# Optimization experiments

Measured on AMD Instinct MI355X. Metric: run time of the kernel, lower is better.

## Reference

```python
import jax, jax.numpy as jnp
from jax import lax
import numpy as np

KS = 3          # kernel_size
PAD = 1         # padding of conv_offset
N = KS * KS     # sampling points per pixel
B, C, H, W = 8, 64, 96, 96
OUTC = 64


def setup_inputs() -> dict:
    key = jax.random.key(0)
    k1, k2, k3 = jax.random.split(key, 3)
    x = jax.random.normal(k1, (B, C, H, W), dtype=jnp.float32)
    # conv_offset: Conv2d(C, 2N, ks=3, pad=1); small init so offsets are modest
    w_off = jax.random.normal(k2, (2 * N, C, KS, KS), dtype=jnp.float32) * 0.01
    b_off = jnp.zeros((2 * N,), jnp.float32)
    # conv_kernel: Conv2d(C, OUTC, ks=3, stride=3)
    w_ker = jax.random.normal(k3, (OUTC, C, KS, KS), dtype=jnp.float32) * (1.0 / np.sqrt(C * KS * KS))
    b_ker = jnp.zeros((OUTC,), jnp.float32)
    return {"x": x, "w_off": w_off, "b_off": b_off, "w_ker": w_ker, "b_ker": b_ker}


def _deform_conv(x, w_off, b_off, w_ker, b_ker):
    b, c, h, w = x.shape
    dn = ('NCHW', 'OIHW', 'NCHW')
    # offset field: (b, 2N, h, w); channels [:N] are x(row) offsets, [N:] are y(col)
    offset = lax.conv_general_dilated(x, w_off, (1, 1), [(PAD, PAD), (PAD, PAD)],
                                      dimension_numbers=dn) + b_off[None, :, None, None]
    r = jnp.arange(-(KS - 1) // 2, (KS - 1) // 2 + 1)
    pnx, pny = jnp.meshgrid(r, r, indexing='ij')          # kernel grid offsets p_n
    gx, gy = jnp.meshgrid(jnp.arange(h), jnp.arange(w), indexing='ij')  # p_0
    px = gx[None, None].astype(x.dtype) + pnx.reshape(1, N, 1, 1).astype(x.dtype) + offset[:, :N]
    py = gy[None, None].astype(x.dtype) + pny.reshape(1, N, 1, 1).astype(x.dtype) + offset[:, N:]
    # Bilinear sampling with zero outside the grid. This is exactly the dense
    # G @ x of the original (only the 4 neighbors of p have nonzero G weight).
    x0 = jnp.floor(px); y0 = jnp.floor(py)
    lx = px - x0; ly = py - y0            # grads flow to offsets through lx/ly
    x0i = lax.stop_gradient(x0).astype(jnp.int32)
    y0i = lax.stop_gradient(y0).astype(jnp.int32)
    x_flat = x.transpose(0, 2, 3, 1).reshape(b, h * w, c)  # (b, HW, c)

    def corner(xi, yi, wt):
        valid = ((xi >= 0) & (xi < h) & (yi >= 0) & (yi < w)).astype(x.dtype)
        idx = (jnp.clip(xi, 0, h - 1) * w + jnp.clip(yi, 0, w - 1)).reshape(b, -1)
        g = jax.vmap(lambda im, ix: im[ix])(x_flat, idx)   # (b, N*h*w, c)
        return g * (wt * valid).reshape(b, -1, 1)

    val = (corner(x0i,     y0i,     (1 - lx) * (1 - ly))
           + corner(x0i + 1, y0i,     lx * (1 - ly))
           + corner(x0i,     y0i + 1, (1 - lx) * ly)
           + corner(x0i + 1, y0i + 1, lx * ly))            # (b, N*h*w, c)
    xo = val.reshape(b, N, h, w, c).transpose(0, 4, 2, 3, 1)        # (b,c,h,w,N)
    # _reshape_x_offset: N -> (kr,kc) tiled into (h*ks, w*ks)
    xo = xo.reshape(b, c, h, w, KS, KS).transpose(0, 1, 2, 4, 3, 5).reshape(b, c, h * KS, w * KS)
    out = lax.conv_general_dilated(xo, w_ker, (KS, KS), 'VALID',
                                   dimension_numbers=dn) + b_ker[None, :, None, None]
    return out  # (b, OUTC, h, w)


def reference(x, w_off, b_off, w_ker, b_ker):
    return _deform_conv(x, w_off, b_off, w_ker, b_ker)
```

## Files before the change

kernel.cpp:

```cpp
#include <hip/hip_runtime.h>

#define H_ 96
#define W_ 96
#define HW 9216
#define C_ 64
#define OUTC 64
#define NPTS 9
#define NCH 18
#define B_ 8
#define NPIX 73728

#define PCH 72

typedef __attribute__((ext_vector_type(8))) short short8;
typedef __attribute__((ext_vector_type(4))) float f32x4;
typedef __attribute__((ext_vector_type(4))) unsigned int uint4v;

__device__ __forceinline__ short f2bf(float f) {
    union { float f; unsigned u; } v; v.f = f;
    unsigned r = v.u + 0x7fffu + ((v.u >> 16) & 1u);
    return (short)(r >> 16);
}
__device__ __forceinline__ float bflo(unsigned d) {
    union { unsigned u; float f; } v; v.u = d << 16; return v.f;
}
__device__ __forceinline__ float bfhi(unsigned d) {
    union { unsigned u; float f; } v; v.u = d & 0xffff0000u; return v.f;
}

__global__ __launch_bounds__(256) void prep_xpose(
    const float* __restrict__ x, const float* __restrict__ w_ker,
    const float* __restrict__ w_off, short* __restrict__ x_t,
    short* __restrict__ wk_frag, short* __restrict__ woff_frag)
{
    int blk = blockIdx.x;
    int t   = threadIdx.x;
    if (blk < 576) {
        int b   = blk & 7;
        int sub = blk >> 3;
        int cb  = t & 7;
        int px  = sub * 128 + (t >> 3) * 4;

        const float* xp = x + ((size_t)(b * C_ + cb * 8) * HW) + px;
        f32x4 tl[8];
#pragma unroll
        for (int e = 0; e < 8; ++e) tl[e] = *(const f32x4*)(xp + (size_t)e * HW);
#pragma unroll
        for (int p = 0; p < 4; ++p) {
            short8 s;
#pragma unroll
            for (int e = 0; e < 8; ++e) s[e] = f2bf(tl[e][p]);
            *(short8*)(x_t + ((size_t)(b * HW + px + p) * 64) + cb * 8) = s;
        }
    } else {
        int idx = (blk - 576) * 256 + t;
        if (idx < 36864) {
            int j = idx & 7, l = (idx >> 3) & 63, nt = (idx >> 9) & 3, sg = idx >> 11;
            int q2 = sg & 1, n = sg >> 1;
            int c  = q2 * 32 + ((l >> 4) << 3) + j;
            int oc = nt * 16 + (l & 15);
            wk_frag[idx] = f2bf(w_ker[(oc * C_ + c) * 9 + n]);
        } else {
            int k = idx - 36864;
            int j = k & 7, l = (k >> 3) & 63, nt = (k >> 9) & 1, sg = k >> 10;
            int q2 = sg & 1, n = sg >> 1;
            int c  = q2 * 32 + ((l >> 4) << 3) + j;
            int oc = nt * 16 + (l & 15);
            woff_frag[k] = (oc < NCH) ? f2bf(w_off[(oc * C_ + c) * 9 + n]) : (short)0;
        }
    }
}

__global__ __launch_bounds__(256, 6) void deform_fused(
    const short* __restrict__ x_t, const short* __restrict__ woff_frag,
    const float* __restrict__ b_off, const short* __restrict__ wk_frag,
    const float* __restrict__ b_ker, float* __restrict__ out)
{
    __shared__ __align__(16) short sX[100 * PCH];
    __shared__ float  sE[64 * 20];
    __shared__ float2 sP[16 * 9];

    int t    = threadIdx.x;
    int lane = t & 63;
    int wv   = t >> 6;
    int b    = blockIdx.x & 7;
    int strip= blockIdx.x >> 3;
    int px0  = strip * 16;
    int i    = px0 / W_;
    int j0   = px0 - i * W_;
    int pxl  = lane & 15, kq = lane >> 4;
    int j    = j0 + pxl;
    const short* xb = x_t + (size_t)b * HW * 64;
    const short8 Z8 = {0,0,0,0,0,0,0,0};

    for (int u = t; u < 800; u += 256) {
        int cb = u & 7, rc = u >> 3;
        int r = rc / 20, c = rc - r * 20;
        int row = min(max(i - 2 + r, 0), H_ - 1);
        int col = min(max(j0 - 2 + c, 0), W_ - 1);
        *(short8*)&sX[rc * PCH + cb * 8] =
            *(const short8*)(xb + (row * W_ + col) * 64 + cb * 8);
    }
    __syncthreads();

    f32x4 pa0 = {0,0,0,0}, pa1 = {0,0,0,0};
    auto p1tap = [&](int n) {
        int di = n / 3 - 1, dj = n % 3 - 1;
        int ii = i + di, jj = j + dj;
        bool ok = (ii >= 0) & (ii < H_) & (jj >= 0) & (jj < W_);
        int rc = (di + 2) * 20 + (pxl + dj + 2);
#pragma unroll
        for (int q2 = 0; q2 < 2; ++q2) {
            short8 a = *(const short8*)&sX[rc * PCH + q2 * 32 + kq * 8];
            a = ok ? a : Z8;
            const short* wb = woff_frag + ((n * 2 + q2) * 2) * 512 + lane * 8;
            short8 b0 = *(const short8*)(wb);
            short8 b1 = *(const short8*)(wb + 512);
            pa0 = __builtin_amdgcn_mfma_f32_16x16x32_bf16(a, b0, pa0, 0, 0, 0);
            pa1 = __builtin_amdgcn_mfma_f32_16x16x32_bf16(a, b1, pa1, 0, 0, 0);
        }
    };
    if      (wv == 0) { p1tap(0); p1tap(1); }
    else if (wv == 1) { p1tap(2); p1tap(3); }
    else if (wv == 2) { p1tap(4); p1tap(5); }
    else              { p1tap(6); p1tap(7); p1tap(8); }
    {
        int col = lane & 15, rq = lane >> 4;
#pragma unroll
        for (int r = 0; r < 4; ++r)
            sE[(wv * 16 + rq * 4 + r) * 20 + col] = pa0[r];
        if (col < 2) {
#pragma unroll
            for (int r = 0; r < 4; ++r)
                sE[(wv * 16 + rq * 4 + r) * 20 + 16 + col] = pa1[r];
        }
    }
    __syncthreads();

    if (t < 144) {
        int p = t / 9, n = t - p * 9;
        float ox = sE[p * 20 + n]             + sE[(16 + p) * 20 + n]
                 + sE[(32 + p) * 20 + n]      + sE[(48 + p) * 20 + n]      + b_off[n];
        float oy = sE[p * 20 + 9 + n]         + sE[(16 + p) * 20 + 9 + n]
                 + sE[(32 + p) * 20 + 9 + n]  + sE[(48 + p) * 20 + 9 + n]  + b_off[9 + n];
        sP[p * 9 + n] = make_float2(ox, oy);
    }
    __syncthreads();

    f32x4 acc[4];
#pragma unroll
    for (int nt = 0; nt < 4; ++nt) acc[nt] = (f32x4){0.f, 0.f, 0.f, 0.f};

    auto p2tap = [&](int n) {
        int di = n / 3 - 1, dj = n % 3 - 1;
        float2 o = sP[pxl * 9 + n];
        float fpx = (float)(i + di) + o.x;
        float fpy = (float)(j + dj) + o.y;
        float x0f = floorf(fpx), y0f = floorf(fpy);
        float lx = fpx - x0f, ly = fpy - y0f;
        int xi = (int)x0f, yi = (int)y0f;
        float wx0 = (xi >= 0  && xi <= H_ - 1) ? (1.0f - lx) : 0.0f;
        float wx1 = (xi >= -1 && xi <= H_ - 2) ? lx          : 0.0f;
        float wy0 = (yi >= 0  && yi <= W_ - 1) ? (1.0f - ly) : 0.0f;
        float wy1 = (yi >= -1 && yi <= W_ - 2) ? ly          : 0.0f;
        float w00 = wx0 * wy0, w10 = wx1 * wy0, w01 = wx0 * wy1, w11 = wx1 * wy1;
        int rp = xi - (i - 2), cp = yi - (j0 - 2);
        bool inp = (rp >= 0) & (rp <= 3) & (cp >= 0) & (cp <= 18);
        uint4v u[8];
        if (inp) {
            int l00 = (rp * 20 + cp) * PCH;
            int l10 = l00 + 20 * PCH, l01 = l00 + PCH, l11 = l10 + PCH;
#pragma unroll
            for (int q2 = 0; q2 < 2; ++q2) {
                int cho = q2 * 32 + kq * 8;
                u[q2*4+0] = *(const uint4v*)&sX[l00 + cho];
                u[q2*4+1] = *(const uint4v*)&sX[l10 + cho];
                u[q2*4+2] = *(const uint4v*)&sX[l01 + cho];
                u[q2*4+3] = *(const uint4v*)&sX[l11 + cho];
            }
        }
        if (!inp) {
            int r0 = min(max(xi,     0), H_ - 1) * W_;
            int r1 = min(max(xi + 1, 0), H_ - 1) * W_;
            int c0 = min(max(yi,     0), W_ - 1);
            int c1 = min(max(yi + 1, 0), W_ - 1);
#pragma unroll
            for (int q2 = 0; q2 < 2; ++q2) {
                int cho = q2 * 32 + kq * 8;
                u[q2*4+0] = *(const uint4v*)(xb + (r0 + c0) * 64 + cho);
                u[q2*4+1] = *(const uint4v*)(xb + (r1 + c0) * 64 + cho);
                u[q2*4+2] = *(const uint4v*)(xb + (r0 + c1) * 64 + cho);
                u[q2*4+3] = *(const uint4v*)(xb + (r1 + c1) * 64 + cho);
            }
        }
#pragma unroll
        for (int q2 = 0; q2 < 2; ++q2) {
            short8 A;
#pragma unroll
            for (int d = 0; d < 4; ++d) {
                float lo = w00 * bflo(u[q2*4+0][d]) + w10 * bflo(u[q2*4+1][d])
                         + w01 * bflo(u[q2*4+2][d]) + w11 * bflo(u[q2*4+3][d]);
                float hi = w00 * bfhi(u[q2*4+0][d]) + w10 * bfhi(u[q2*4+1][d])
                         + w01 * bfhi(u[q2*4+2][d]) + w11 * bfhi(u[q2*4+3][d]);
                A[2 * d]     = f2bf(lo);
                A[2 * d + 1] = f2bf(hi);
            }
            const short* wbp = wk_frag + ((n * 2 + q2) * 4) * 512 + lane * 8;
#pragma unroll
            for (int nt = 0; nt < 4; ++nt) {
                short8 bfr = *(const short8*)(wbp + nt * 512);
                acc[nt] = __builtin_amdgcn_mfma_f32_16x16x32_bf16(A, bfr, acc[nt], 0, 0, 0);
            }
        }
    };
    if      (wv == 0) { p2tap(0); p2tap(1); }
    else if (wv == 1) { p2tap(2); p2tap(3); }
    else if (wv == 2) { p2tap(4); p2tap(5); }
    else              { p2tap(6); p2tap(7); p2tap(8); }

    __syncthreads();
    int col = lane & 15, rq = lane >> 4;
    if (wv == 0) {
#pragma unroll
        for (int nt = 0; nt < 4; ++nt) {
            int oc = nt * 16 + col;
            float bias = b_ker[oc];
#pragma unroll
            for (int r = 0; r < 4; ++r)
                sE[oc * 20 + rq * 4 + r] = acc[nt][r] + bias;
        }
    }
    __syncthreads();
    if (wv == 1) {
#pragma unroll
        for (int nt = 0; nt < 4; ++nt) {
            int oc = nt * 16 + col;
#pragma unroll
            for (int r = 0; r < 4; ++r)
                sE[oc * 20 + rq * 4 + r] += acc[nt][r];
        }
    }
    __syncthreads();
    if (wv == 2) {
#pragma unroll
        for (int nt = 0; nt < 4; ++nt) {
            int oc = nt * 16 + col;
#pragma unroll
            for (int r = 0; r < 4; ++r)
                sE[oc * 20 + rq * 4 + r] += acc[nt][r];
        }
    }
    __syncthreads();
    if (wv == 3) {
#pragma unroll
        for (int nt = 0; nt < 4; ++nt) {
            int oc = nt * 16 + col;
#pragma unroll
            for (int r = 0; r < 4; ++r)
                sE[oc * 20 + rq * 4 + r] += acc[nt][r];
        }
    }
    __syncthreads();

    int oc = t >> 2, qr = t & 3;
    const float* se = &sE[oc * 20 + qr * 4];
    float* outp = out + ((size_t)(b * OUTC + oc) * HW) + px0 + qr * 4;
    *(f32x4*)outp = *(const f32x4*)se;
}

extern "C" void kernel_launch(void* const* d_in, const int* in_sizes, int n_in,
                              void* d_out, int out_size, void* d_ws, size_t ws_size,
                              hipStream_t stream) {
    const float* x     = (const float*)d_in[0];
    const float* w_off = (const float*)d_in[1];
    const float* b_off = (const float*)d_in[2];
    const float* w_ker = (const float*)d_in[3];
    const float* b_ker = (const float*)d_in[4];
    float* out = (float*)d_out;

    char*  wsb       = (char*)d_ws;
    short* x_t       = (short*)wsb;
    short* wk_frag   = (short*)(wsb + 9437184);
    short* woff_frag = wk_frag + 36864;

    prep_xpose  <<<792,  256, 0, stream>>>(x, w_ker, w_off, x_t, wk_frag, woff_frag);
    deform_fused<<<4608, 256, 0, stream>>>(x_t, woff_frag, b_off, wk_frag, b_ker, out);
}
```

Measured before the change: 109.8 us.

## Assign one output row per wave over 4x16 tiles, dropping cross-wave tap reduction

```diff
diff --git a/kernel.cpp b/kernel.cpp
--- a/kernel.cpp
+++ b/kernel.cpp
@@ -8,7 +8,6 @@
 #define NPTS 9
 #define NCH 18
 #define B_ 8
-#define NPIX 73728
 
 #define PCH 72
 
@@ -71,32 +70,35 @@
     }
 }
 
-__global__ __launch_bounds__(256, 6) void deform_fused(
+__global__ __launch_bounds__(256, 5) void deform_fused(
     const short* __restrict__ x_t, const short* __restrict__ woff_frag,
     const float* __restrict__ b_off, const short* __restrict__ wk_frag,
     const float* __restrict__ b_ker, float* __restrict__ out)
 {
-    __shared__ __align__(16) short sX[100 * PCH];
-    __shared__ float  sE[64 * 20];
-    __shared__ float2 sP[16 * 9];
+    __shared__ __align__(16) short sX[160 * PCH];
+    __shared__ float2 sP[4][16][9];
 
     int t    = threadIdx.x;
     int lane = t & 63;
     int wv   = t >> 6;
     int b    = blockIdx.x & 7;
-    int strip= blockIdx.x >> 3;
-    int px0  = strip * 16;
-    int i    = px0 / W_;
-    int j0   = px0 - i * W_;
+    int s    = blockIdx.x >> 3;
+    int rg   = s / 6;
+    int cs   = s - rg * 6;
+    int i0   = rg * 4;
+    int j0   = cs * 16;
     int pxl  = lane & 15, kq = lane >> 4;
+    int iw   = i0 + wv;
     int j    = j0 + pxl;
     const short* xb = x_t + (size_t)b * HW * 64;
     const short8 Z8 = {0,0,0,0,0,0,0,0};
 
-    for (int u = t; u < 800; u += 256) {
+#pragma unroll
+    for (int k = 0; k < 5; ++k) {
+        int u  = t + k * 256;
         int cb = u & 7, rc = u >> 3;
         int r = rc / 20, c = rc - r * 20;
-        int row = min(max(i - 2 + r, 0), H_ - 1);
+        int row = min(max(i0 - 2 + r, 0), H_ - 1);
         int col = min(max(j0 - 2 + c, 0), W_ - 1);
         *(short8*)&sX[rc * PCH + cb * 8] =
             *(const short8*)(xb + (row * W_ + col) * 64 + cb * 8);
@@ -104,14 +106,14 @@
     __syncthreads();
 
     f32x4 pa0 = {0,0,0,0}, pa1 = {0,0,0,0};
-    auto p1tap = [&](int n) {
+#pragma unroll
+    for (int n = 0; n < 9; ++n) {
         int di = n / 3 - 1, dj = n % 3 - 1;
-        int ii = i + di, jj = j + dj;
-        bool ok = (ii >= 0) & (ii < H_) & (jj >= 0) & (jj < W_);
-        int rc = (di + 2) * 20 + (pxl + dj + 2);
+        bool ok = ((unsigned)(iw + di) < (unsigned)H_) & ((unsigned)(j + dj) < (unsigned)W_);
+        int rcb = ((wv + di + 2) * 20 + (pxl + dj + 2)) * PCH;
 #pragma unroll
         for (int q2 = 0; q2 < 2; ++q2) {
-            short8 a = *(const short8*)&sX[rc * PCH + q2 * 32 + kq * 8];
+            short8 a = *(const short8*)&sX[rcb + q2 * 32 + kq * 8];
             a = ok ? a : Z8;
             const short* wb = woff_frag + ((n * 2 + q2) * 2) * 512 + lane * 8;
             short8 b0 = *(const short8*)(wb);
@@ -119,42 +121,33 @@
             pa0 = __builtin_amdgcn_mfma_f32_16x16x32_bf16(a, b0, pa0, 0, 0, 0);
             pa1 = __builtin_amdgcn_mfma_f32_16x16x32_bf16(a, b1, pa1, 0, 0, 0);
         }
-    };
-    if      (wv == 0) { p1tap(0); p1tap(1); }
-    else if (wv == 1) { p1tap(2); p1tap(3); }
-    else if (wv == 2) { p1tap(4); p1tap(5); }
-    else              { p1tap(6); p1tap(7); p1tap(8); }
+    }
     {
         int col = lane & 15, rq = lane >> 4;
-#pragma unroll
-        for (int r = 0; r < 4; ++r)
-            sE[(wv * 16 + rq * 4 + r) * 20 + col] = pa0[r];
+        float bo = b_off[col];
+        if (col < 9) {
+#pragma unroll
+            for (int r = 0; r < 4; ++r) sP[wv][rq * 4 + r][col].x = pa0[r] + bo;
+        } else {
+#pragma unroll
+            for (int r = 0; r < 4; ++r) sP[wv][rq * 4 + r][col - 9].y = pa0[r] + bo;
+        }
         if (col < 2) {
-#pragma unroll
-            for (int r = 0; r < 4; ++r)
-                sE[(wv * 16 + rq * 4 + r) * 20 + 16 + col] = pa1[r];
-        }
-    }
-    __syncthreads();
-
-    if (t < 144) {
-        int p = t / 9, n = t - p * 9;
-        float ox = sE[p * 20 + n]             + sE[(16 + p) * 20 + n]
-                 + sE[(32 + p) * 20 + n]      + sE[(48 + p) * 20 + n]      + b_off[n];
-        float oy = sE[p * 20 + 9 + n]         + sE[(16 + p) * 20 + 9 + n]
-                 + sE[(32 + p) * 20 + 9 + n]  + sE[(48 + p) * 20 + 9 + n]  + b_off[9 + n];
-        sP[p * 9 + n] = make_float2(ox, oy);
-    }
-    __syncthreads();
+            float bo2 = b_off[16 + col];
+#pragma unroll
+            for (int r = 0; r < 4; ++r) sP[wv][rq * 4 + r][7 + col].y = pa1[r] + bo2;
+        }
+    }
 
     f32x4 acc[4];
 #pragma unroll
     for (int nt = 0; nt < 4; ++nt) acc[nt] = (f32x4){0.f, 0.f, 0.f, 0.f};
 
-    auto p2tap = [&](int n) {
+#pragma unroll
+    for (int n = 0; n < 9; ++n) {
         int di = n / 3 - 1, dj = n % 3 - 1;
-        float2 o = sP[pxl * 9 + n];
-        float fpx = (float)(i + di) + o.x;
+        float2 o = sP[wv][pxl][n];
+        float fpx = (float)(iw + di) + o.x;
         float fpy = (float)(j + dj) + o.y;
         float x0f = floorf(fpx), y0f = floorf(fpy);
         float lx = fpx - x0f, ly = fpy - y0f;
@@ -164,8 +157,8 @@
         float wy0 = (yi >= 0  && yi <= W_ - 1) ? (1.0f - ly) : 0.0f;
         float wy1 = (yi >= -1 && yi <= W_ - 2) ? ly          : 0.0f;
         float w00 = wx0 * wy0, w10 = wx1 * wy0, w01 = wx0 * wy1, w11 = wx1 * wy1;
-        int rp = xi - (i - 2), cp = yi - (j0 - 2);
-        bool inp = (rp >= 0) & (rp <= 3) & (cp >= 0) & (cp <= 18);
+        int rp = xi - (i0 - 2), cp = yi - (j0 - 2);
+        bool inp = (rp >= 0) & (rp <= 6) & (cp >= 0) & (cp <= 18);
         uint4v u[8];
         if (inp) {
             int l00 = (rp * 20 + cp) * PCH;
@@ -212,60 +205,31 @@
                 acc[nt] = __builtin_amdgcn_mfma_f32_16x16x32_bf16(A, bfr, acc[nt], 0, 0, 0);
             }
         }
-    };
-    if      (wv == 0) { p2tap(0); p2tap(1); }
-    else if (wv == 1) { p2tap(2); p2tap(3); }
-    else if (wv == 2) { p2tap(4); p2tap(5); }
-    else              { p2tap(6); p2tap(7); p2tap(8); }
+    }
 
     __syncthreads();
-    int col = lane & 15, rq = lane >> 4;
-    if (wv == 0) {
+    float* fw = (float*)sX + wv * 1280;
+    {
+        int col = lane & 15, rq = lane >> 4;
 #pragma unroll
         for (int nt = 0; nt < 4; ++nt) {
             int oc = nt * 16 + col;
             float bias = b_ker[oc];
 #pragma unroll
             for (int r = 0; r < 4; ++r)
-                sE[oc * 20 + rq * 4 + r] = acc[nt][r] + bias;
-        }
-    }
-    __syncthreads();
-    if (wv == 1) {
-#pragma unroll
-        for (int nt = 0; nt < 4; ++nt) {
-            int oc = nt * 16 + col;
-#pragma unroll
-            for (int r = 0; r < 4; ++r)
-                sE[oc * 20 + rq * 4 + r] += acc[nt][r];
-        }
-    }
-    __syncthreads();
-    if (wv == 2) {
-#pragma unroll
-        for (int nt = 0; nt < 4; ++nt) {
-            int oc = nt * 16 + col;
-#pragma unroll
-            for (int r = 0; r < 4; ++r)
-                sE[oc * 20 + rq * 4 + r] += acc[nt][r];
-        }
-    }
-    __syncthreads();
-    if (wv == 3) {
-#pragma unroll
-        for (int nt = 0; nt < 4; ++nt) {
-            int oc = nt * 16 + col;
-#pragma unroll
-            for (int r = 0; r < 4; ++r)
-                sE[oc * 20 + rq * 4 + r] += acc[nt][r];
-        }
-    }
-    __syncthreads();
-
-    int oc = t >> 2, qr = t & 3;
-    const float* se = &sE[oc * 20 + qr * 4];
-    float* outp = out + ((size_t)(b * OUTC + oc) * HW) + px0 + qr * 4;
-    *(f32x4*)outp = *(const f32x4*)se;
+                fw[oc * 20 + rq * 4 + r] = acc[nt][r] + bias;
+        }
+    }
+    {
+        int ocl = lane >> 2, qq = lane & 3;
+        float* ob = out + (size_t)b * OUTC * HW + iw * W_ + j0 + qq * 4;
+#pragma unroll
+        for (int it = 0; it < 4; ++it) {
+            int oc = it * 16 + ocl;
+            f32x4 v = *(const f32x4*)&fw[oc * 20 + qq * 4];
+            *(f32x4*)(ob + (size_t)oc * HW) = v;
+        }
+    }
 }
 
 extern "C" void kernel_launch(void* const* d_in, const int* in_sizes, int n_in,
@@ -284,5 +248,5 @@
     short* woff_frag = wk_frag + 36864;
 
     prep_xpose  <<<792,  256, 0, stream>>>(x, w_ker, w_off, x_t, wk_frag, woff_frag);
-    deform_fused<<<4608, 256, 0, stream>>>(x_t, woff_frag, b_off, wk_frag, b_ker, out);
-}
+    deform_fused<<<1152, 256, 0, stream>>>(x_t, woff_frag, b_off, wk_frag, b_ker, out);
+}
```

Result: faster. 105.9 us (-3.6%).
